# Kernel tuning notes

Hardware: AMD Instinct MI355X
Metric: run time of the kernel (lower is better)

## Reference

```python
import jax, jax.numpy as jnp
import numpy as np

NUM_WIRES = 18
NUM_LAYERS = 3
BATCH = 64
DIM = 2 ** NUM_WIRES


def _apply_ry(psi, theta, w):
    # RY(t) = [[cos(t/2), -sin(t/2)], [sin(t/2), cos(t/2)]] on wire w (wire 0 = MSB)
    B = psi.shape[0]
    c = jnp.cos(theta * 0.5).astype(psi.dtype)
    s = jnp.sin(theta * 0.5).astype(psi.dtype)
    p = psi.reshape(B, 2 ** w, 2, -1)
    a, b = p[:, :, 0], p[:, :, 1]
    return jnp.stack([c * a - s * b, s * a + c * b], axis=2).reshape(B, -1)


def _apply_rz(psi, theta, w):
    # RZ(t) = diag(e^{-i t/2}, e^{+i t/2}) on wire w
    B = psi.shape[0]
    half = (theta * 0.5).astype(jnp.complex64)
    p0 = jnp.exp(-1j * half)
    p1 = jnp.exp(1j * half)
    p = psi.reshape(B, 2 ** w, 2, -1)
    return jnp.stack([p0 * p[:, :, 0], p1 * p[:, :, 1]], axis=2).reshape(B, -1)


def _apply_cnot_adjacent(psi, w):
    # CNOT with control w, target w+1: flip target bit where control bit = 1
    B = psi.shape[0]
    p = psi.reshape(B, 2 ** w, 2, 2, -1)
    p = p.at[:, :, 1].set(p[:, :, 1, ::-1])
    return p.reshape(B, -1)


def _expval_z(psi, w):
    # <Z_w> = P(bit_w = 0) - P(bit_w = 1)
    B = psi.shape[0]
    prob = (psi.real ** 2 + psi.imag ** 2).reshape(B, 2 ** w, 2, -1)
    p = prob.sum(axis=(1, 3))  # (B, 2)
    return p[:, 0] - p[:, 1]


def _circuit(psi, params):
    for layer in range(params.shape[0]):
        for w in range(NUM_WIRES):
            psi = _apply_ry(psi, params[layer, 0, w], w)
            psi = _apply_rz(psi, params[layer, 1, w], w)
        for w in range(NUM_WIRES - 1):
            psi = _apply_cnot_adjacent(psi, w)
    # expvals of PauliZ on every wire -> (B, num_wires)
    return jnp.stack([_expval_z(psi, w) for w in range(NUM_WIRES)], axis=-1)


def setup_inputs() -> dict:
    key = jax.random.key(0)
    k1, k2, k3, k4, k5 = jax.random.split(key, 5)
    state_re = jax.random.normal(k1, (BATCH, DIM), dtype=jnp.float32)
    state_im = jax.random.normal(k2, (BATCH, DIM), dtype=jnp.float32)
    norm = jnp.sqrt(jnp.sum(state_re ** 2 + state_im ** 2, axis=-1, keepdims=True))
    state_re = state_re / norm
    state_im = state_im / norm
    params = jax.random.normal(k3, (NUM_LAYERS, 2, NUM_WIRES), dtype=jnp.float32)
    head_w = jax.random.normal(k4, (1, NUM_WIRES), dtype=jnp.float32) / np.sqrt(NUM_WIRES)
    head_b = jax.random.normal(k5, (1,), dtype=jnp.float32) / np.sqrt(NUM_WIRES)
    return {"state_re": state_re, "state_im": state_im, "params": params,
            "head_w": head_w, "head_b": head_b}


def reference(state_re, state_im, params, head_w, head_b):
    psi = (state_re + 1j * state_im).astype(jnp.complex64)  # (B, 2^n)
    feats = _circuit(psi, params)                            # (B, n)
    out = feats @ head_w.T + head_b                          # (B, 1)
    return out[:, 0]
```

## Files before the change

### kernel.cpp

```cpp
#include <hip/hip_runtime.h>


static __device__ __forceinline__ int phys(int m) {
    return m + 4 * ((m >> 6) + (m >> 9));
}

template<int J>
__device__ __forceinline__ void sqg(float* ar, float* ai, float c, float s, float pc, float ps) {
#pragma unroll
    for (int r = 0; r < 32; ++r) {
        if (((r >> J) & 1) == 0) {
            const int r1 = r + (1 << J);
            const float a0r = ar[r], a0i = ai[r], a1r = ar[r1], a1i = ai[r1];
            ar[r] = fmaf(c, a0r, -(s * a1r));
            ai[r] = fmaf(c, a0i, -(s * a1i));
            const float t1r = fmaf(s, a0r, c * a1r);
            const float t1i = fmaf(s, a0i, c * a1i);
            ar[r1] = fmaf(pc, t1r, -(ps * t1i));
            ai[r1] = fmaf(pc, t1i,  (ps * t1r));
        }
    }
}

template<int JC, int JT>
__device__ __forceinline__ void cnotg(float* ar, float* ai) {
#pragma unroll
    for (int r = 0; r < 32; ++r) {
        if (((r >> JC) & 1) == 1 && ((r >> JT) & 1) == 0) {
            const int r1 = r + (1 << JT);
            float tr = ar[r]; ar[r] = ar[r1]; ar[r1] = tr;
            float ti = ai[r]; ai[r] = ai[r1]; ai[r1] = ti;
        }
    }
}

__global__ __launch_bounds__(128) void passB_k(float* __restrict__ re, float* __restrict__ im,
                                               const float* __restrict__ params, int layer)
{
    __shared__ float lre[4384], lim[4384];
    const int t    = threadIdx.x;
    const int b    = blockIdx.x >> 6;
    const int mid  = blockIdx.x & 63;
    const int base = (b << 18) | (mid << 5);

    float C[7], S[7], PC[7], PS[7];
    const float* pl = params + layer * 36;
#pragma unroll
    for (int k = 0; k < 7; ++k) {
        const int w = 6 - k;
        __sincosf(0.5f * pl[w], &S[k], &C[k]);
        __sincosf(pl[18 + w], &PS[k], &PC[k]);
    }

    float ar[32], ai[32];
#pragma unroll
    for (int r = 0; r < 32; ++r) {
        const int n = base + (r << 13) + ((t >> 5) << 11) + (t & 31);
        ar[r] = re[n]; ai[r] = im[n];
    }
    sqg<4>(ar, ai, C[6], S[6], PC[6], PS[6]);
    sqg<3>(ar, ai, C[5], S[5], PC[5], PS[5]);
    sqg<2>(ar, ai, C[4], S[4], PC[4], PS[4]);
    sqg<1>(ar, ai, C[3], S[3], PC[3], PS[3]);
    sqg<0>(ar, ai, C[2], S[2], PC[2], PS[2]);
    cnotg<4,3>(ar, ai);
    cnotg<3,2>(ar, ai);
    cnotg<2,1>(ar, ai);
    cnotg<1,0>(ar, ai);

#pragma unroll
    for (int r = 0; r < 32; ++r) {
        const int m = (r << 7) | t;
        lre[phys(m)] = ar[r]; lim[phys(m)] = ai[r];
    }
    __syncthreads();
#pragma unroll
    for (int g = 0; g < 8; ++g) {
        const int m = ((t >> 3) << 8) | (g << 5) | ((t & 7) << 2);
        const float4 vr = *(const float4*)&lre[phys(m)];
        const float4 vi = *(const float4*)&lim[phys(m)];
        ar[4*g+0] = vr.x; ar[4*g+1] = vr.y; ar[4*g+2] = vr.z; ar[4*g+3] = vr.w;
        ai[4*g+0] = vi.x; ai[4*g+1] = vi.y; ai[4*g+2] = vi.z; ai[4*g+3] = vi.w;
    }
    sqg<3>(ar, ai, C[1], S[1], PC[1], PS[1]);
    sqg<2>(ar, ai, C[0], S[0], PC[0], PS[0]);
    cnotg<4,3>(ar, ai);
    cnotg<3,2>(ar, ai);

#pragma unroll
    for (int g = 0; g < 8; ++g) {
        const int n = base + ((t >> 3) << 14) + (g << 11) + ((t & 7) << 2);
        *(float4*)&re[n] = make_float4(ar[4*g+0], ar[4*g+1], ar[4*g+2], ar[4*g+3]);
        *(float4*)&im[n] = make_float4(ai[4*g+0], ai[4*g+1], ai[4*g+2], ai[4*g+3]);
    }
}

template<bool FINAL>
__global__ __launch_bounds__(128) void passA_k(float* __restrict__ re, float* __restrict__ im,
                                               const float* __restrict__ params, int layer,
                                               const float* __restrict__ hw,
                                               const float* __restrict__ hb,
                                               float* __restrict__ out)
{
    __shared__ float lre[4384], lim[4384];
    const int t    = threadIdx.x;
    const int b    = blockIdx.x >> 6;
    const int hi   = blockIdx.x & 63;
    const int base = (b << 18) | (hi << 12);

    float C[11], S[11], PC[11], PS[11];
    const float* pl = params + layer * 36;
#pragma unroll
    for (int p = 0; p < 11; ++p) {
        const int w = 17 - p;
        __sincosf(0.5f * pl[w], &S[p], &C[p]);
        __sincosf(pl[18 + w], &PS[p], &PC[p]);
    }

    float ar[32], ai[32];
#pragma unroll
    for (int r = 0; r < 32; ++r) {
        const int n = base + (r << 7) + t;
        ar[r] = re[n]; ai[r] = im[n];
    }
    sqg<3>(ar, ai, C[10], S[10], PC[10], PS[10]);
    sqg<2>(ar, ai, C[9],  S[9],  PC[9],  PS[9]);
    sqg<1>(ar, ai, C[8],  S[8],  PC[8],  PS[8]);
    sqg<0>(ar, ai, C[7],  S[7],  PC[7],  PS[7]);
    cnotg<4,3>(ar, ai); cnotg<3,2>(ar, ai); cnotg<2,1>(ar, ai); cnotg<1,0>(ar, ai);

#pragma unroll
    for (int r = 0; r < 32; ++r) {
        const int m = (r << 7) | t;
        lre[phys(m)] = ar[r]; lim[phys(m)] = ai[r];
    }
    __syncthreads();
#pragma unroll
    for (int r = 0; r < 32; ++r) {
        const int m = ((t >> 3) << 8) | (r << 3) | (t & 7);
        ar[r] = lre[phys(m)]; ai[r] = lim[phys(m)];
    }
    sqg<3>(ar, ai, C[6], S[6], PC[6], PS[6]);
    sqg<2>(ar, ai, C[5], S[5], PC[5], PS[5]);
    sqg<1>(ar, ai, C[4], S[4], PC[4], PS[4]);
    sqg<0>(ar, ai, C[3], S[3], PC[3], PS[3]);
    cnotg<4,3>(ar, ai); cnotg<3,2>(ar, ai); cnotg<2,1>(ar, ai); cnotg<1,0>(ar, ai);

    __syncthreads();
#pragma unroll
    for (int r = 0; r < 32; ++r) {
        const int m = ((t >> 3) << 8) | (r << 3) | (t & 7);
        lre[phys(m)] = ar[r]; lim[phys(m)] = ai[r];
    }
    __syncthreads();
#pragma unroll
    for (int g = 0; g < 8; ++g) {
        const int m = (t << 5) | (g << 2);
        const float4 vr = *(const float4*)&lre[phys(m)];
        const float4 vi = *(const float4*)&lim[phys(m)];
        ar[4*g+0] = vr.x; ar[4*g+1] = vr.y; ar[4*g+2] = vr.z; ar[4*g+3] = vr.w;
        ai[4*g+0] = vi.x; ai[4*g+1] = vi.y; ai[4*g+2] = vi.z; ai[4*g+3] = vi.w;
    }
    sqg<2>(ar, ai, C[2], S[2], PC[2], PS[2]);
    sqg<1>(ar, ai, C[1], S[1], PC[1], PS[1]);
    sqg<0>(ar, ai, C[0], S[0], PC[0], PS[0]);
    cnotg<3,2>(ar, ai); cnotg<2,1>(ar, ai); cnotg<1,0>(ar, ai);

    if (!FINAL) {
        __syncthreads();
#pragma unroll
        for (int g = 0; g < 8; ++g) {
            const int m = (t << 5) | (g << 2);
            *(float4*)&lre[phys(m)] = make_float4(ar[4*g+0], ar[4*g+1], ar[4*g+2], ar[4*g+3]);
            *(float4*)&lim[phys(m)] = make_float4(ai[4*g+0], ai[4*g+1], ai[4*g+2], ai[4*g+3]);
        }
        __syncthreads();
#pragma unroll
        for (int g = 0; g < 8; ++g) {
            const int m = (g << 9) | (t << 2);
            const float4 vr = *(const float4*)&lre[phys(m)];
            const float4 vi = *(const float4*)&lim[phys(m)];
            const int n = base + (g << 9) + (t << 2);
            *(float4*)&re[n] = vr;
            *(float4*)&im[n] = vi;
        }
    } else {
        float accP = 0.f, D0 = 0.f, D1 = 0.f, D2 = 0.f, D3 = 0.f, D4 = 0.f;
#pragma unroll
        for (int r = 0; r < 32; ++r) {
            const float p = ar[r] * ar[r] + ai[r] * ai[r];
            accP += p;
            if (r & 1)  D0 -= p; else D0 += p;
            if (r & 2)  D1 -= p; else D1 += p;
            if (r & 4)  D2 -= p; else D2 += p;
            if (r & 8)  D3 -= p; else D3 += p;
            if (r & 16) D4 -= p; else D4 += p;
        }
        float G = 0.f;
#pragma unroll
        for (int k = 0; k < 7; ++k)
            G += ((t >> k) & 1) ? -hw[12 - k] : hw[12 - k];
#pragma unroll
        for (int k = 0; k < 6; ++k)
            G += ((hi >> k) & 1) ? -hw[5 - k] : hw[5 - k];
        float v = accP * G + D0 * hw[17] + D1 * hw[16] + D2 * hw[15] + D3 * hw[14] + D4 * hw[13];
        if (t == 0 && hi == 0) v += hb[0];
#pragma unroll
        for (int off = 32; off > 0; off >>= 1) v += __shfl_xor(v, off);
        if ((t & 63) == 0) atomicAdd(&out[b], v);
    }
}

extern "C" void kernel_launch(void* const* d_in, const int* in_sizes, int n_in,
                              void* d_out, int out_size, void* d_ws, size_t ws_size,
                              hipStream_t stream)
{
    float* re            = (float*)d_in[0];
    float* im            = (float*)d_in[1];
    const float* params  = (const float*)d_in[2];
    const float* hw      = (const float*)d_in[3];
    const float* hb      = (const float*)d_in[4];
    float* out           = (float*)d_out;
    (void)in_sizes; (void)n_in; (void)d_ws; (void)ws_size;

    hipMemsetAsync(out, 0, (size_t)out_size * sizeof(float), stream);

    const dim3 grid(4096), blk(128);
    for (int l = 0; l < 3; ++l) {
        passB_k<<<grid, blk, 0, stream>>>(re, im, params, l);
        if (l < 2) passA_k<false><<<grid, blk, 0, stream>>>(re, im, params, l, nullptr, nullptr, nullptr);
        else       passA_k<true ><<<grid, blk, 0, stream>>>(re, im, params, l, hw, hb, out);
    }
}
```

Baseline: 447.0 us.

## Restructure passes to per-wavefront tiles with folded CNOT permutations and shuffles

```diff
diff --git a/kernel.cpp b/kernel.cpp
--- a/kernel.cpp
+++ b/kernel.cpp
@@ -1,8 +1,11 @@
 #include <hip/hip_runtime.h>
 
 
-static __device__ __forceinline__ int phys(int m) {
-    return m + 4 * ((m >> 6) + (m >> 9));
+#define LROW 36u
+#define LDSW 2304u
+
+static __device__ __forceinline__ float rfl(float x) {
+    return __int_as_float(__builtin_amdgcn_readfirstlane(__float_as_int(x)));
 }
 
 template<int J>
@@ -22,74 +25,98 @@
     }
 }
 
-template<int JC, int JT>
-__device__ __forceinline__ void cnotg(float* ar, float* ai) {
-#pragma unroll
-    for (int r = 0; r < 32; ++r) {
-        if (((r >> JC) & 1) == 1 && ((r >> JT) & 1) == 0) {
-            const int r1 = r + (1 << JT);
-            float tr = ar[r]; ar[r] = ar[r1]; ar[r1] = tr;
-            float ti = ai[r]; ai[r] = ai[r1]; ai[r1] = ti;
-        }
-    }
-}
-
 __global__ __launch_bounds__(128) void passB_k(float* __restrict__ re, float* __restrict__ im,
                                                const float* __restrict__ params, int layer)
 {
-    __shared__ float lre[4384], lim[4384];
-    const int t    = threadIdx.x;
-    const int b    = blockIdx.x >> 6;
-    const int mid  = blockIdx.x & 63;
-    const int base = (b << 18) | (mid << 5);
+    __shared__ float lds[2 * LDSW];
+    const int t   = threadIdx.x;
+    const int l   = t & 63;
+    const int wib = t >> 6;
+    float* Lb = lds + wib * LDSW;
+    const int wv  = (blockIdx.x << 1) | wib;
+    const int b   = wv >> 7;
+    const int mid = wv & 127;
+    const int L5 = (l >> 5) & 1, L4 = (l >> 4) & 1, L3 = (l >> 3) & 1, L2 = (l >> 2) & 1;
+    const int L1 = (l >> 1) & 1, L0 = l & 1;
+
+    const unsigned base = ((unsigned)b << 18) | ((unsigned)mid << 4);
+    const unsigned sel  = (L5 << 17) | (L4 << 16) | (L3 << 12) | (L2 << 11) | (L1 << 3) | (L0 << 2);
 
     float C[7], S[7], PC[7], PS[7];
     const float* pl = params + layer * 36;
 #pragma unroll
     for (int k = 0; k < 7; ++k) {
         const int w = 6 - k;
-        __sincosf(0.5f * pl[w], &S[k], &C[k]);
-        __sincosf(pl[18 + w], &PS[k], &PC[k]);
+        float sv, cv;
+        __sincosf(0.5f * pl[w], &sv, &cv);  S[k] = rfl(sv);  C[k] = rfl(cv);
+        __sincosf(pl[18 + w], &sv, &cv);    PS[k] = rfl(sv); PC[k] = rfl(cv);
     }
 
     float ar[32], ai[32];
 #pragma unroll
-    for (int r = 0; r < 32; ++r) {
-        const int n = base + (r << 13) + ((t >> 5) << 11) + (t & 31);
-        ar[r] = re[n]; ai[r] = im[n];
-    }
+    for (int g = 0; g < 8; ++g) {
+        const unsigned n = base + sel + ((unsigned)g << 13);
+        const float4 vr = *(const float4*)&re[n];
+        const float4 vi = *(const float4*)&im[n];
+        ar[4*g+0] = vr.x; ar[4*g+1] = vr.y; ar[4*g+2] = vr.z; ar[4*g+3] = vr.w;
+        ai[4*g+0] = vi.x; ai[4*g+1] = vi.y; ai[4*g+2] = vi.z; ai[4*g+3] = vi.w;
+    }
+
+    sqg<4>(ar, ai, C[4], S[4], PC[4], PS[4]);
+    sqg<3>(ar, ai, C[3], S[3], PC[3], PS[3]);
+    sqg<2>(ar, ai, C[2], S[2], PC[2], PS[2]);
+
+    const unsigned tb = (unsigned)L0 * 144u + (unsigned)(l >> 1);
+#pragma unroll
+    for (int g = 0; g < 8; ++g)
+#pragma unroll
+        for (int c = 0; c < 4; ++c)
+            Lb[tb + g * 288 + c * 36] = ar[4*g+c];
+#pragma unroll
+    for (int q = 0; q < 8; ++q) {
+        const float4 v = *(const float4*)&Lb[(unsigned)l * LROW + (q << 2)];
+        ar[4*q+0] = v.x; ar[4*q+1] = v.y; ar[4*q+2] = v.z; ar[4*q+3] = v.w;
+    }
+#pragma unroll
+    for (int g = 0; g < 8; ++g)
+#pragma unroll
+        for (int c = 0; c < 4; ++c)
+            Lb[tb + g * 288 + c * 36] = ai[4*g+c];
+#pragma unroll
+    for (int q = 0; q < 8; ++q) {
+        const float4 v = *(const float4*)&Lb[(unsigned)l * LROW + (q << 2)];
+        ai[4*q+0] = v.x; ai[4*q+1] = v.y; ai[4*q+2] = v.z; ai[4*q+3] = v.w;
+    }
+
     sqg<4>(ar, ai, C[6], S[6], PC[6], PS[6]);
     sqg<3>(ar, ai, C[5], S[5], PC[5], PS[5]);
-    sqg<2>(ar, ai, C[4], S[4], PC[4], PS[4]);
-    sqg<1>(ar, ai, C[3], S[3], PC[3], PS[3]);
-    sqg<0>(ar, ai, C[2], S[2], PC[2], PS[2]);
-    cnotg<4,3>(ar, ai);
-    cnotg<3,2>(ar, ai);
-    cnotg<2,1>(ar, ai);
-    cnotg<1,0>(ar, ai);
-
-#pragma unroll
-    for (int r = 0; r < 32; ++r) {
-        const int m = (r << 7) | t;
-        lre[phys(m)] = ar[r]; lim[phys(m)] = ai[r];
-    }
-    __syncthreads();
+    sqg<2>(ar, ai, C[1], S[1], PC[1], PS[1]);
+    sqg<1>(ar, ai, C[0], S[0], PC[0], PS[0]);
+
+#pragma unroll
+    for (int q = 0; q < 8; ++q)
+        *(float4*)&Lb[(unsigned)l * LROW + (q << 2)] =
+            make_float4(ar[4*q+0], ar[4*q+1], ar[4*q+2], ar[4*q+3]);
+#pragma unroll
+    for (int g = 0; g < 8; ++g)
+#pragma unroll
+        for (int c = 0; c < 4; ++c)
+            ar[4*g+c] = Lb[tb + g * 288 + c * 36];
+#pragma unroll
+    for (int q = 0; q < 8; ++q)
+        *(float4*)&Lb[(unsigned)l * LROW + (q << 2)] =
+            make_float4(ai[4*q+0], ai[4*q+1], ai[4*q+2], ai[4*q+3]);
+#pragma unroll
+    for (int g = 0; g < 8; ++g)
+#pragma unroll
+        for (int c = 0; c < 4; ++c)
+            ai[4*g+c] = Lb[tb + g * 288 + c * 36];
+
 #pragma unroll
     for (int g = 0; g < 8; ++g) {
-        const int m = ((t >> 3) << 8) | (g << 5) | ((t & 7) << 2);
-        const float4 vr = *(const float4*)&lre[phys(m)];
-        const float4 vi = *(const float4*)&lim[phys(m)];
-        ar[4*g+0] = vr.x; ar[4*g+1] = vr.y; ar[4*g+2] = vr.z; ar[4*g+3] = vr.w;
-        ai[4*g+0] = vi.x; ai[4*g+1] = vi.y; ai[4*g+2] = vi.z; ai[4*g+3] = vi.w;
-    }
-    sqg<3>(ar, ai, C[1], S[1], PC[1], PS[1]);
-    sqg<2>(ar, ai, C[0], S[0], PC[0], PS[0]);
-    cnotg<4,3>(ar, ai);
-    cnotg<3,2>(ar, ai);
-
-#pragma unroll
-    for (int g = 0; g < 8; ++g) {
-        const int n = base + ((t >> 3) << 14) + (g << 11) + ((t & 7) << 2);
+        int h = (L5 << 6) | (L4 << 5) | (g << 2) | (L3 << 1) | L2;
+        int x = h ^ (h >> 1); x ^= x >> 2; x ^= x >> 4;
+        const unsigned n = base + ((unsigned)x << 11) + (L1 << 3) + (L0 << 2);
         *(float4*)&re[n] = make_float4(ar[4*g+0], ar[4*g+1], ar[4*g+2], ar[4*g+3]);
         *(float4*)&im[n] = make_float4(ai[4*g+0], ai[4*g+1], ai[4*g+2], ai[4*g+3]);
     }
@@ -102,112 +129,158 @@
                                                const float* __restrict__ hb,
                                                float* __restrict__ out)
 {
-    __shared__ float lre[4384], lim[4384];
-    const int t    = threadIdx.x;
-    const int b    = blockIdx.x >> 6;
-    const int hi   = blockIdx.x & 63;
-    const int base = (b << 18) | (hi << 12);
+    __shared__ float lds[2 * LDSW];
+    const int t   = threadIdx.x;
+    const int l   = t & 63;
+    const int wib = t >> 6;
+    float* Lb = lds + wib * LDSW;
+    const int wv  = (blockIdx.x << 1) | wib;
+    const int b   = wv >> 7;
+    const int hi7 = wv & 127;
+    const int n11 = hi7 & 1;
+    const unsigned base = ((unsigned)b << 18) | ((unsigned)hi7 << 11);
 
     float C[11], S[11], PC[11], PS[11];
     const float* pl = params + layer * 36;
 #pragma unroll
-    for (int p = 0; p < 11; ++p) {
-        const int w = 17 - p;
-        __sincosf(0.5f * pl[w], &S[p], &C[p]);
-        __sincosf(pl[18 + w], &PS[p], &PC[p]);
+    for (int k = 0; k < 11; ++k) {
+        const int w = 17 - k;
+        float sv, cv;
+        __sincosf(0.5f * pl[w], &sv, &cv);  S[k] = rfl(sv);  C[k] = rfl(cv);
+        __sincosf(pl[18 + w], &sv, &cv);    PS[k] = rfl(sv); PC[k] = rfl(cv);
     }
 
     float ar[32], ai[32];
 #pragma unroll
-    for (int r = 0; r < 32; ++r) {
-        const int n = base + (r << 7) + t;
-        ar[r] = re[n]; ai[r] = im[n];
-    }
-    sqg<3>(ar, ai, C[10], S[10], PC[10], PS[10]);
-    sqg<2>(ar, ai, C[9],  S[9],  PC[9],  PS[9]);
-    sqg<1>(ar, ai, C[8],  S[8],  PC[8],  PS[8]);
-    sqg<0>(ar, ai, C[7],  S[7],  PC[7],  PS[7]);
-    cnotg<4,3>(ar, ai); cnotg<3,2>(ar, ai); cnotg<2,1>(ar, ai); cnotg<1,0>(ar, ai);
-
-#pragma unroll
-    for (int r = 0; r < 32; ++r) {
-        const int m = (r << 7) | t;
-        lre[phys(m)] = ar[r]; lim[phys(m)] = ai[r];
-    }
-    __syncthreads();
-#pragma unroll
-    for (int r = 0; r < 32; ++r) {
-        const int m = ((t >> 3) << 8) | (r << 3) | (t & 7);
-        ar[r] = lre[phys(m)]; ai[r] = lim[phys(m)];
-    }
-    sqg<3>(ar, ai, C[6], S[6], PC[6], PS[6]);
-    sqg<2>(ar, ai, C[5], S[5], PC[5], PS[5]);
-    sqg<1>(ar, ai, C[4], S[4], PC[4], PS[4]);
-    sqg<0>(ar, ai, C[3], S[3], PC[3], PS[3]);
-    cnotg<4,3>(ar, ai); cnotg<3,2>(ar, ai); cnotg<2,1>(ar, ai); cnotg<1,0>(ar, ai);
-
-    __syncthreads();
-#pragma unroll
-    for (int r = 0; r < 32; ++r) {
-        const int m = ((t >> 3) << 8) | (r << 3) | (t & 7);
-        lre[phys(m)] = ar[r]; lim[phys(m)] = ai[r];
-    }
-    __syncthreads();
-#pragma unroll
     for (int g = 0; g < 8; ++g) {
-        const int m = (t << 5) | (g << 2);
-        const float4 vr = *(const float4*)&lre[phys(m)];
-        const float4 vi = *(const float4*)&lim[phys(m)];
+        const unsigned n = base + ((unsigned)g << 8) + ((unsigned)l << 2);
+        const float4 vr = *(const float4*)&re[n];
+        const float4 vi = *(const float4*)&im[n];
         ar[4*g+0] = vr.x; ar[4*g+1] = vr.y; ar[4*g+2] = vr.z; ar[4*g+3] = vr.w;
         ai[4*g+0] = vi.x; ai[4*g+1] = vi.y; ai[4*g+2] = vi.z; ai[4*g+3] = vi.w;
     }
-    sqg<2>(ar, ai, C[2], S[2], PC[2], PS[2]);
-    sqg<1>(ar, ai, C[1], S[1], PC[1], PS[1]);
-    sqg<0>(ar, ai, C[0], S[0], PC[0], PS[0]);
-    cnotg<3,2>(ar, ai); cnotg<2,1>(ar, ai); cnotg<1,0>(ar, ai);
+
+    sqg<4>(ar, ai, C[10], S[10], PC[10], PS[10]);
+    sqg<3>(ar, ai, C[9],  S[9],  PC[9],  PS[9]);
+    sqg<2>(ar, ai, C[8],  S[8],  PC[8],  PS[8]);
+    sqg<1>(ar, ai, C[1],  S[1],  PC[1],  PS[1]);
+    sqg<0>(ar, ai, C[0],  S[0],  PC[0],  PS[0]);
+
+    {
+        const int side   = (l >> 5) & 1;
+        const float c7   = C[7];
+        const float bco  = side ? S[7] : -S[7];
+        const float qc   = side ? PC[7] : 1.f;
+        const float qs   = side ? PS[7] : 0.f;
+#pragma unroll
+        for (int r = 0; r < 32; ++r) {
+            const float pr = __shfl_xor(ar[r], 32);
+            const float pi = __shfl_xor(ai[r], 32);
+            const float tr = fmaf(c7, ar[r], bco * pr);
+            const float ti = fmaf(c7, ai[r], bco * pi);
+            ar[r] = fmaf(qc, tr, -(qs * ti));
+            ai[r] = fmaf(qc, ti,  (qs * tr));
+        }
+    }
+
+    const unsigned tb = (unsigned)((l >> 5) & 1) * 144u + (unsigned)(l & 31);
+#pragma unroll
+    for (int g = 0; g < 8; ++g)
+#pragma unroll
+        for (int c = 0; c < 4; ++c)
+            Lb[tb + g * 288 + c * 36] = ar[4*g+c];
+#pragma unroll
+    for (int q = 0; q < 8; ++q) {
+        const float4 v = *(const float4*)&Lb[(unsigned)l * LROW + (q << 2)];
+        ar[4*q+0] = v.x; ar[4*q+1] = v.y; ar[4*q+2] = v.z; ar[4*q+3] = v.w;
+    }
+#pragma unroll
+    for (int g = 0; g < 8; ++g)
+#pragma unroll
+        for (int c = 0; c < 4; ++c)
+            Lb[tb + g * 288 + c * 36] = ai[4*g+c];
+#pragma unroll
+    for (int q = 0; q < 8; ++q) {
+        const float4 v = *(const float4*)&Lb[(unsigned)l * LROW + (q << 2)];
+        ai[4*q+0] = v.x; ai[4*q+1] = v.y; ai[4*q+2] = v.z; ai[4*q+3] = v.w;
+    }
+
+    sqg<4>(ar, ai, C[6], S[6], PC[6], PS[6]);
+    sqg<3>(ar, ai, C[5], S[5], PC[5], PS[5]);
+    sqg<2>(ar, ai, C[4], S[4], PC[4], PS[4]);
+    sqg<1>(ar, ai, C[3], S[3], PC[3], PS[3]);
+    sqg<0>(ar, ai, C[2], S[2], PC[2], PS[2]);
+
+#pragma unroll
+    for (int q = 0; q < 8; ++q)
+        *(float4*)&Lb[(unsigned)l * LROW + (q << 2)] =
+            make_float4(ar[4*q+0], ar[4*q+1], ar[4*q+2], ar[4*q+3]);
+#pragma unroll
+    for (int g = 0; g < 8; ++g)
+#pragma unroll
+        for (int c = 0; c < 4; ++c)
+            ar[4*g+c] = Lb[tb + g * 288 + c * 36];
+#pragma unroll
+    for (int q = 0; q < 8; ++q)
+        *(float4*)&Lb[(unsigned)l * LROW + (q << 2)] =
+            make_float4(ai[4*q+0], ai[4*q+1], ai[4*q+2], ai[4*q+3]);
+#pragma unroll
+    for (int g = 0; g < 8; ++g)
+#pragma unroll
+        for (int c = 0; c < 4; ++c)
+            ai[4*g+c] = Lb[tb + g * 288 + c * 36];
+
+    const int msk = n11 ? 0x1FF : 0;
 
     if (!FINAL) {
-        __syncthreads();
 #pragma unroll
         for (int g = 0; g < 8; ++g) {
-            const int m = (t << 5) | (g << 2);
-            *(float4*)&lre[phys(m)] = make_float4(ar[4*g+0], ar[4*g+1], ar[4*g+2], ar[4*g+3]);
-            *(float4*)&lim[phys(m)] = make_float4(ai[4*g+0], ai[4*g+1], ai[4*g+2], ai[4*g+3]);
-        }
-        __syncthreads();
+            int h = (g << 6) | l;
+            int x = h ^ (h >> 1); x ^= x >> 2; x ^= x >> 4; x ^= x >> 8;
+            x ^= msk;
+            const int y = x & 1;
+            const float r0 = ar[4*g+0], r1 = ar[4*g+1], r2 = ar[4*g+2], r3 = ar[4*g+3];
+            const float i0 = ai[4*g+0], i1 = ai[4*g+1], i2 = ai[4*g+2], i3 = ai[4*g+3];
+            float4 sr, si;
+            sr.x = y ? r2 : r0;  sr.y = y ? r3 : r1;  sr.z = y ? r1 : r3;  sr.w = y ? r0 : r2;
+            si.x = y ? i2 : i0;  si.y = y ? i3 : i1;  si.z = y ? i1 : i3;  si.w = y ? i0 : i2;
+            const unsigned n = base + ((unsigned)x << 2);
+            *(float4*)&re[n] = sr;
+            *(float4*)&im[n] = si;
+        }
+    } else {
+        float Ghi = 0.f;
+#pragma unroll
+        for (int j = 0; j < 7; ++j) {
+            const float wv_ = hw[6 - j];
+            Ghi += ((hi7 >> j) & 1) ? -wv_ : wv_;
+        }
+        float acc = 0.f;
 #pragma unroll
         for (int g = 0; g < 8; ++g) {
-            const int m = (g << 9) | (t << 2);
-            const float4 vr = *(const float4*)&lre[phys(m)];
-            const float4 vi = *(const float4*)&lim[phys(m)];
-            const int n = base + (g << 9) + (t << 2);
-            *(float4*)&re[n] = vr;
-            *(float4*)&im[n] = vi;
-        }
-    } else {
-        float accP = 0.f, D0 = 0.f, D1 = 0.f, D2 = 0.f, D3 = 0.f, D4 = 0.f;
-#pragma unroll
-        for (int r = 0; r < 32; ++r) {
-            const float p = ar[r] * ar[r] + ai[r] * ai[r];
-            accP += p;
-            if (r & 1)  D0 -= p; else D0 += p;
-            if (r & 2)  D1 -= p; else D1 += p;
-            if (r & 4)  D2 -= p; else D2 += p;
-            if (r & 8)  D3 -= p; else D3 += p;
-            if (r & 16) D4 -= p; else D4 += p;
-        }
-        float G = 0.f;
-#pragma unroll
-        for (int k = 0; k < 7; ++k)
-            G += ((t >> k) & 1) ? -hw[12 - k] : hw[12 - k];
-#pragma unroll
-        for (int k = 0; k < 6; ++k)
-            G += ((hi >> k) & 1) ? -hw[5 - k] : hw[5 - k];
-        float v = accP * G + D0 * hw[17] + D1 * hw[16] + D2 * hw[15] + D3 * hw[14] + D4 * hw[13];
-        if (t == 0 && hi == 0) v += hb[0];
-#pragma unroll
-        for (int off = 32; off > 0; off >>= 1) v += __shfl_xor(v, off);
-        if ((t & 63) == 0) atomicAdd(&out[b], v);
+            int h = (g << 6) | l;
+            int x = h ^ (h >> 1); x ^= x >> 2; x ^= x >> 4; x ^= x >> 8;
+            x ^= msk;
+            const float q0 = fmaf(ar[4*g+0], ar[4*g+0], ai[4*g+0] * ai[4*g+0]);
+            const float q1 = fmaf(ar[4*g+1], ar[4*g+1], ai[4*g+1] * ai[4*g+1]);
+            const float q2 = fmaf(ar[4*g+2], ar[4*g+2], ai[4*g+2] * ai[4*g+2]);
+            const float q3 = fmaf(ar[4*g+3], ar[4*g+3], ai[4*g+3] * ai[4*g+3]);
+            const float psum = (q0 + q1) + (q2 + q3);
+            const float d1   = (q0 + q1) - (q2 + q3);
+            const float d0   = (q0 - q1) - (q2 - q3);
+            float Gm = 0.f;
+#pragma unroll
+            for (int j = 0; j < 9; ++j) {
+                const float wv_ = hw[15 - j];
+                Gm += ((x >> j) & 1) ? -wv_ : wv_;
+            }
+            const float ys = (x & 1) ? -1.f : 1.f;
+            acc += psum * (Ghi + Gm) + ys * fmaf(d1, hw[16], d0 * hw[17]);
+        }
+        if (hi7 == 0 && l == 0) acc += hb[0];
+#pragma unroll
+        for (int off = 32; off > 0; off >>= 1) acc += __shfl_xor(acc, off);
+        if (l == 0) atomicAdd(&out[b], acc);
     }
 }
 
@@ -215,12 +288,12 @@
                               void* d_out, int out_size, void* d_ws, size_t ws_size,
                               hipStream_t stream)
 {
-    float* re            = (float*)d_in[0];
-    float* im            = (float*)d_in[1];
-    const float* params  = (const float*)d_in[2];
-    const float* hw      = (const float*)d_in[3];
-    const float* hb      = (const float*)d_in[4];
-    float* out           = (float*)d_out;
+    float* re           = (float*)d_in[0];
+    float* im           = (float*)d_in[1];
+    const float* params = (const float*)d_in[2];
+    const float* hw     = (const float*)d_in[3];
+    const float* hb     = (const float*)d_in[4];
+    float* out          = (float*)d_out;
     (void)in_sizes; (void)n_in; (void)d_ws; (void)ws_size;
 
     hipMemsetAsync(out, 0, (size_t)out_size * sizeof(float), stream);
```

Result: slower. 458.7 us (+2.6%).
